# Kernel tuning notes

Measured on AMD Instinct MI355X. Metric: run time of the kernel, lower is better.

## Reference

```python
import math
import jax, jax.numpy as jnp
import numpy as np

D_MODEL, N_HEADS, QKV, D_HEAD, D_FF, N_BLOCKS, IN_DIM = 288, 8, 328, 41, 1315, 4, 83
B, S = 1024, 128
EPS = 1e-5


def setup_inputs() -> dict:
    key = jax.random.key(0)
    ks = iter(jax.random.split(key, 64))
    def rn(shape, scale=0.05):
        return jax.random.normal(next(ks), shape, jnp.float32) * scale
    inp = {
        "x": jax.random.normal(next(ks), (B, S, IN_DIM), jnp.float32),
        "Wp": rn((D_MODEL, IN_DIM)), "bp": rn((D_MODEL,)),
        "phase": rn((D_MODEL,)),
        "Wq": rn((N_BLOCKS, QKV, D_MODEL)), "bq": rn((N_BLOCKS, QKV)),
        "Wk": rn((N_BLOCKS, QKV, D_MODEL)), "bk": rn((N_BLOCKS, QKV)),
        "Wv": rn((N_BLOCKS, QKV, D_MODEL)), "bv": rn((N_BLOCKS, QKV)),
        "Wo": rn((N_BLOCKS, D_MODEL, QKV)), "bo": rn((N_BLOCKS, D_MODEL)),
        "temp": jnp.ones((N_BLOCKS,), jnp.float32) + rn((N_BLOCKS,), 0.01),
        "qscale": jnp.ones((N_BLOCKS, N_HEADS), jnp.float32) + rn((N_BLOCKS, N_HEADS), 0.01),
        "Wf1": rn((N_BLOCKS, D_FF, D_MODEL)), "bf1": rn((N_BLOCKS, D_FF)),
        "Wf2": rn((N_BLOCKS, D_MODEL, D_FF)), "bf2": rn((N_BLOCKS, D_MODEL)),
        "n1w": jnp.ones((N_BLOCKS, D_MODEL), jnp.float32), "n1b": jnp.zeros((N_BLOCKS, D_MODEL), jnp.float32),
        "n2w": jnp.ones((N_BLOCKS, D_MODEL), jnp.float32), "n2b": jnp.zeros((N_BLOCKS, D_MODEL), jnp.float32),
        "skip": jnp.ones((N_BLOCKS,), jnp.float32),
        "bn_w": jnp.ones((D_MODEL,), jnp.float32), "bn_b": jnp.zeros((D_MODEL,), jnp.float32),
        "bn_mean": rn((D_MODEL,)), "bn_var": jax.random.uniform(next(ks), (D_MODEL,), jnp.float32, 0.5, 1.5),
        "h1w": rn((144, D_MODEL)), "h1b": rn((144,)),
        "h2w": rn((72, 144)), "h2b": rn((72,)),
        "h3w": rn((1, 72)), "h3b": rn((1,)),
        "u1w": rn((72, D_MODEL)), "u1b": rn((72,)),
        "u2w": rn((1, 72)), "u2b": rn((1,)),
    }
    return inp


def _layer_norm(x, w, b):
    mu = jnp.mean(x, axis=-1, keepdims=True)
    var = jnp.mean((x - mu) ** 2, axis=-1, keepdims=True)
    return (x - mu) * jax.lax.rsqrt(var + EPS) * w + b


def reference(x, Wp, bp, phase, Wq, bq, Wk, bk, Wv, bv, Wo, bo, temp, qscale,
              Wf1, bf1, Wf2, bf2, n1w, n1b, n2w, n2b, skip,
              bn_w, bn_b, bn_mean, bn_var,
              h1w, h1b, h2w, h2b, h3w, h3b, u1w, u1b, u2w, u2b):
    Bsz, Sl, _ = x.shape
    # input projection
    h = jnp.einsum('bsi,di->bsd', x, Wp) + bp
    # sinusoidal positional encoding modulated by cos(quantum_phase)
    pos = jnp.arange(Sl, dtype=jnp.float32)[:, None]
    div = jnp.exp(jnp.arange(0, D_MODEL, 2, dtype=jnp.float32) * (-math.log(10000.0) / D_MODEL))
    pe = jnp.zeros((Sl, D_MODEL), jnp.float32)
    pe = pe.at[:, 0::2].set(jnp.sin(pos * div)).at[:, 1::2].set(jnp.cos(pos * div))
    h = h + pe * jnp.cos(phase)

    for l in range(N_BLOCKS):
        # attention with temperature-scaled softmax + post-softmax per-head scale
        q = (jnp.einsum('bsd,qd->bsq', h, Wq[l]) + bq[l]).reshape(Bsz, Sl, N_HEADS, D_HEAD)
        k = (jnp.einsum('bsd,qd->bsq', h, Wk[l]) + bk[l]).reshape(Bsz, Sl, N_HEADS, D_HEAD)
        v = (jnp.einsum('bsd,qd->bsq', h, Wv[l]) + bv[l]).reshape(Bsz, Sl, N_HEADS, D_HEAD)
        scale = math.sqrt(D_HEAD) * temp[l]
        scores = jnp.einsum('bqhd,bkhd->bhqk', q, k) / scale  # [B,H,S,S]
        attn = jax.nn.softmax(scores, axis=-1) * qscale[l][None, :, None, None]
        o = jnp.einsum('bhqk,bkhd->bqhd', attn, v).reshape(Bsz, Sl, QKV)
        o = jnp.einsum('bsq,dq->bsd', o, Wo[l]) + bo[l]
        h = _layer_norm(h + skip[l] * o, n1w[l], n1b[l])
        # GELU FFN (exact erf gelu, dropout inactive in eval)
        f = jax.nn.gelu(jnp.einsum('bsd,fd->bsf', h, Wf1[l]) + bf1[l], approximate=False)
        f = jnp.einsum('bsf,df->bsd', f, Wf2[l]) + bf2[l]
        h = _layer_norm(h + f, n2w[l], n2b[l])

    pooled = jnp.mean(h, axis=1)  # [B, D_MODEL]
    # output head: BatchNorm1d (eval, running stats) -> GELU -> MLP
    z = (pooled - bn_mean) * jax.lax.rsqrt(bn_var + EPS) * bn_w + bn_b
    z = jax.nn.gelu(z, approximate=False)
    z = jax.nn.gelu(z @ h1w.T + h1b, approximate=False)
    z = jax.nn.gelu(z @ h2w.T + h2b, approximate=False)
    pred = z @ h3w.T + h3b  # [B, 1]
    # uncertainty head
    u = jax.nn.relu(pooled @ u1w.T + u1b)
    unc = jax.nn.softplus(u @ u2w.T + u2b)  # [B, 1]
    return pred, unc
```

## Files before the change

### kernel.cpp

```cpp
#include <hip/hip_runtime.h>
#include <cstdint>

typedef __attribute__((ext_vector_type(8))) short short8;
typedef __attribute__((ext_vector_type(4))) short s4v;
typedef __attribute__((ext_vector_type(4))) float floatx4;

#define DEV __device__ __forceinline__

DEV short f2bf(float f) {
  unsigned u = __builtin_bit_cast(unsigned, f);
  u += 0x7fffu + ((u >> 16) & 1u);
  return (short)(u >> 16);
}
DEV short f2bf_ru(float f) {
  unsigned u = __builtin_bit_cast(unsigned, f);
  return (short)((u + 0x8000u) >> 16);
}
DEV float bf2f(short s) {
  unsigned u = ((unsigned)(unsigned short)s) << 16;
  return __builtin_bit_cast(float, u);
}
DEV float gelu_exact(float x) {
  return 0.5f * x * (1.0f + erff(x * 0.70710678118654752f));
}
DEV float gelu_fast(float x) {
  const float t2 = 1.5957691216057308f * (x + 0.044715f * x * x * x);
  return x / (1.0f + __expf(-t2));
}
DEV void gload16(const void* g, void* l) {
  __builtin_amdgcn_global_load_lds((const __attribute__((address_space(1))) void*)g,
                                   (__attribute__((address_space(3))) void*)l,
                                   16, 0, 0);
}

template<int MODE>
__global__ __launch_bounds__(256)
void gemm_kernel(const short* __restrict__ A, const short* __restrict__ Bw,
                 const float* __restrict__ bias, short* __restrict__ C,
                 const float* __restrict__ pe,
                 int K, int lda, int ldb, int ldc, int Nstore, int NT, long hstride)
{
  __shared__ __align__(16) short lds[128 * 136];
  short* Ct = lds;

  const int tid  = threadIdx.x;
  const int wave = tid >> 6, lane = tid & 63;
  const int quad = lane >> 4, r16 = lane & 15;
  const int per = gridDim.x >> 3;
  const int gti = (blockIdx.x & 7) * per + (blockIdx.x >> 3);
  const int mt = gti / NT, nt = gti - mt * NT;
  const int wm = (wave >> 1) * 64, wn = (wave & 1) * 64;

  const long Abase = (long)mt * 128 * lda;
  const long Bbase = (long)nt * 128 * ldb;

  floatx4 acc[4][4] = {};

  int k0 = 0;
  for (; k0 + 64 <= K; k0 += 64) {
    __syncthreads();
#pragma unroll
    for (int j = 0; j < 8; ++j) {
      const int c2 = tid + j * 256;
      const int op = c2 >> 10;
      const int cb = c2 & 1023;
      const int half = cb >> 9;
      const int sub = cb & 511;
      const int row = sub >> 2, cc = (sub & 3) ^ ((row >> 1) & 3);
      const short* src = op ? (Bw + Bbase + (long)row * ldb + k0 + half * 32 + cc * 8)
                            : (A  + Abase + (long)row * lda + k0 + half * 32 + cc * 8);
      gload16(src, &lds[(size_t)(op * 8192 + half * 4096 + (sub & ~63) * 8)]);
    }
    __syncthreads();

#pragma unroll
    for (int s = 0; s < 2; ++s) {
      short8 af[4], bfr[4];
#pragma unroll
      for (int i = 0; i < 4; ++i) {
        const int R = wm + i * 16 + r16;
        af[i] = *(const short8*)&lds[s * 4096 + R * 32 + (quad ^ ((R >> 1) & 3)) * 8];
      }
#pragma unroll
      for (int j = 0; j < 4; ++j) {
        const int R = wn + j * 16 + r16;
        bfr[j] = *(const short8*)&lds[8192 + s * 4096 + R * 32 + (quad ^ ((R >> 1) & 3)) * 8];
      }
#pragma unroll
      for (int i = 0; i < 4; ++i)
#pragma unroll
        for (int j = 0; j < 4; ++j)
          acc[i][j] = __builtin_amdgcn_mfma_f32_16x16x32_bf16(bfr[j], af[i], acc[i][j], 0, 0, 0);
    }
  }

  if (k0 < K) {
    short* As = lds;
    short* Bs = lds + 128 * 32;
    const int row0 = tid >> 2,         cc0 = (tid & 3) ^ ((row0 >> 1) & 3);
    const int row1 = (256 + tid) >> 2, cc1 = ((256 + tid) & 3) ^ ((row1 >> 1) & 3);
    __syncthreads();
    gload16(A  + Abase + (long)row0 * lda + k0 + cc0 * 8, &As[(0 * 256 + wave * 64) * 8]);
    gload16(A  + Abase + (long)row1 * lda + k0 + cc1 * 8, &As[(1 * 256 + wave * 64) * 8]);
    gload16(Bw + Bbase + (long)row0 * ldb + k0 + cc0 * 8, &Bs[(0 * 256 + wave * 64) * 8]);
    gload16(Bw + Bbase + (long)row1 * ldb + k0 + cc1 * 8, &Bs[(1 * 256 + wave * 64) * 8]);
    __syncthreads();

    short8 af[4], bfr[4];
#pragma unroll
    for (int i = 0; i < 4; ++i) {
      const int R = wm + i * 16 + r16;
      af[i] = *(const short8*)&As[R * 32 + (quad ^ ((R >> 1) & 3)) * 8];
    }
#pragma unroll
    for (int j = 0; j < 4; ++j) {
      const int R = wn + j * 16 + r16;
      bfr[j] = *(const short8*)&Bs[R * 32 + (quad ^ ((R >> 1) & 3)) * 8];
    }
#pragma unroll
    for (int i = 0; i < 4; ++i)
#pragma unroll
      for (int j = 0; j < 4; ++j)
        acc[i][j] = __builtin_amdgcn_mfma_f32_16x16x32_bf16(bfr[j], af[i], acc[i][j], 0, 0, 0);
  }

  const int mb0 = mt * 128, tb = nt * 128;

  __syncthreads();
#pragma unroll
  for (int j = 0; j < 4; ++j) {
    const int n0 = wn + j * 16 + quad * 4;
    const floatx4 b4 = *(const floatx4*)&bias[tb + n0];
#pragma unroll
    for (int i = 0; i < 4; ++i) {
      const int m = wm + i * 16 + r16;
      floatx4 v = acc[i][j] + b4;
      if (MODE == 1) {
#pragma unroll
        for (int rg = 0; rg < 4; ++rg) v[rg] = gelu_fast(v[rg]);
      }
      if (MODE == 2) {
        const floatx4 p4 = *(const floatx4*)&pe[((mb0 + m) & 127) * 384 + tb + n0];
        v = v + p4;
      }
      s4v o4;
#pragma unroll
      for (int rg = 0; rg < 4; ++rg) o4[rg] = f2bf_ru(v[rg]);
      *(s4v*)&Ct[m * 136 + n0] = o4;
    }
  }
  __syncthreads();

#pragma unroll
  for (int rr = 0; rr < 8; ++rr) {
    const int chunk = rr * 256 + tid;
    const int row = chunk >> 4, ch = chunk & 15;
    const int gcol = tb + ch * 8;
    if (MODE == 3) {
      const int g = gcol / 48, d0 = gcol - g * 48;
      *(short8*)(C + (long)g * hstride + (long)(mb0 + row) * 48 + d0) =
          *(const short8*)&Ct[row * 136 + ch * 8];
    } else if (gcol < Nstore) {
      *(short8*)(C + (long)(mb0 + row) * ldc + gcol) = *(const short8*)&Ct[row * 136 + ch * 8];
    }
  }
}

template<bool AHEAD>
__global__ __launch_bounds__(512, 4)
void gemm_ln_kernel(const short* __restrict__ A, const short* __restrict__ Bw,
                    const float* __restrict__ bias, short* __restrict__ h,
                    const float* __restrict__ lnw, const float* __restrict__ lnb,
                    const float* __restrict__ skip_p, int layer, int use_skip,
                    int K, int lda, int ldb, long ahs)
{
  __shared__ __align__(16) short lds[128 * 296];
  __shared__ float redp[4][2][2][16];
  __shared__ float reds[4][2][2][16];
  short* Hs = lds;

  const int tid  = threadIdx.x;
  const int wave = tid >> 6, lane = tid & 63;
  const int quad = lane >> 4, r16 = lane & 15;
  const int wr = wave >> 1, wc = wave & 1;
  const int mt = blockIdx.x;
  const long mrow0 = (long)mt * 128;

  floatx4 acc[2][9] = {};

  auto stage = [&](short* buf, int k0) {
    for (int c = tid; c < 1664; c += 512) {
      const void* src;
      if (c < 512) {
        const int row = c >> 2, cc = (c & 3) ^ ((row >> 1) & 3);
        if (AHEAD) {
          const int kc = k0 + cc * 8;
          const int g = kc / 48, d = kc - g * 48;
          src = A + (long)g * ahs + (mrow0 + row) * 48 + d;
        } else {
          src = A + (mrow0 + row) * lda + k0 + cc * 8;
        }
      } else {
        const int cb = c - 512;
        const int row = cb >> 2, cc = (cb & 3) ^ ((row >> 1) & 3);
        src = Bw + (long)row * ldb + k0 + cc * 8;
      }
      gload16(src, &buf[(size_t)(c & ~63) * 8]);
    }
  };

  auto compute = [&](const short* buf) {
    const short* As_ = buf;
    const short* Bs_ = buf + 4096;
    const int Ra0 = wr * 32 + r16, Ra1 = Ra0 + 16;
    const short8 af0 = *(const short8*)&As_[Ra0 * 32 + (quad ^ ((Ra0 >> 1) & 3)) * 8];
    const short8 af1 = *(const short8*)&As_[Ra1 * 32 + (quad ^ ((Ra1 >> 1) & 3)) * 8];
#pragma unroll
    for (int t = 0; t < 9; ++t) {
      const int Rb = wc * 144 + t * 16 + r16;
      const short8 b = *(const short8*)&Bs_[Rb * 32 + (quad ^ ((Rb >> 1) & 3)) * 8];
      acc[0][t] = __builtin_amdgcn_mfma_f32_16x16x32_bf16(b, af0, acc[0][t], 0, 0, 0);
      acc[1][t] = __builtin_amdgcn_mfma_f32_16x16x32_bf16(b, af1, acc[1][t], 0, 0, 0);
    }
  };

  short* const B0 = lds;
  short* const B1 = lds + 13312;

  stage(B0, 0);
  __syncthreads();
  int k0 = 0;
  while (true) {
    if (k0 + 32 < K) stage(B1, k0 + 32);
    compute(B0);
    __syncthreads();
    k0 += 32;
    if (k0 >= K) break;
    if (k0 + 32 < K) stage(B0, k0 + 32);
    compute(B1);
    __syncthreads();
    k0 += 32;
    if (k0 >= K) break;
  }

  for (int c = tid; c < 4608; c += 512) {
    const int row = c / 36, ch = c - row * 36;
    *(short8*)&Hs[row * 296 + ch * 8] =
        *(const short8*)(h + (mrow0 + row) * 288 + ch * 8);
  }
  __syncthreads();

  const float skipv = use_skip ? skip_p[layer] : 1.0f;
  const int m0 = wr * 32 + r16, m1 = m0 + 16;

  float ps0 = 0.f, ss0 = 0.f, ps1 = 0.f, ss1 = 0.f;
#pragma unroll
  for (int t = 0; t < 9; ++t) {
    const int n0 = wc * 144 + t * 16 + quad * 4;
    const floatx4 b4 = *(const floatx4*)&bias[n0];
    const s4v h40 = *(const s4v*)&Hs[m0 * 296 + n0];
    const s4v h41 = *(const s4v*)&Hs[m1 * 296 + n0];
#pragma unroll
    for (int rg = 0; rg < 4; ++rg) {
      const float y0 = bf2f(h40[rg]) + skipv * (acc[0][t][rg] + b4[rg]);
      const float y1 = bf2f(h41[rg]) + skipv * (acc[1][t][rg] + b4[rg]);
      acc[0][t][rg] = y0; acc[1][t][rg] = y1;
      ps0 += y0; ss0 += y0 * y0;
      ps1 += y1; ss1 += y1 * y1;
    }
  }
  ps0 += __shfl_xor(ps0, 16); ps0 += __shfl_xor(ps0, 32);
  ss0 += __shfl_xor(ss0, 16); ss0 += __shfl_xor(ss0, 32);
  ps1 += __shfl_xor(ps1, 16); ps1 += __shfl_xor(ps1, 32);
  ss1 += __shfl_xor(ss1, 16); ss1 += __shfl_xor(ss1, 32);
  if (lane < 16) {
    redp[wr][wc][0][r16] = ps0; redp[wr][wc][1][r16] = ps1;
    reds[wr][wc][0][r16] = ss0; reds[wr][wc][1][r16] = ss1;
  }
  __syncthreads();
  const float psum0 = redp[wr][0][0][r16] + redp[wr][1][0][r16];
  const float psum1 = redp[wr][0][1][r16] + redp[wr][1][1][r16];
  const float ssum0 = reds[wr][0][0][r16] + reds[wr][1][0][r16];
  const float ssum1 = reds[wr][0][1][r16] + reds[wr][1][1][r16];
  const float mean0 = psum0 * (1.f / 288.f), mean1 = psum1 * (1.f / 288.f);
  const float rstd0 = rsqrtf(ssum0 * (1.f / 288.f) - mean0 * mean0 + 1e-5f);
  const float rstd1 = rsqrtf(ssum1 * (1.f / 288.f) - mean1 * mean1 + 1e-5f);

#pragma unroll
  for (int t = 0; t < 9; ++t) {
    const int n0 = wc * 144 + t * 16 + quad * 4;
    const floatx4 w4 = *(const floatx4*)&lnw[n0];
    const floatx4 l4 = *(const floatx4*)&lnb[n0];
    s4v o0, o1;
#pragma unroll
    for (int rg = 0; rg < 4; ++rg) {
      o0[rg] = f2bf_ru((acc[0][t][rg] - mean0) * rstd0 * w4[rg] + l4[rg]);
      o1[rg] = f2bf_ru((acc[1][t][rg] - mean1) * rstd1 * w4[rg] + l4[rg]);
    }
    *(s4v*)&Hs[m0 * 296 + n0] = o0;
    *(s4v*)&Hs[m1 * 296 + n0] = o1;
  }
  __syncthreads();

  for (int c = tid; c < 4608; c += 512) {
    const int row = c / 36, ch = c - row * 36;
    *(short8*)(h + (mrow0 + row) * 288 + ch * 8) =
        *(const short8*)&Hs[row * 296 + ch * 8];
  }
}

__global__ __launch_bounds__(512, 2)
void ffn_kernel(short* __restrict__ h,
                const short* __restrict__ W1, const float* __restrict__ b1,
                const short* __restrict__ W2, const float* __restrict__ b2,
                const float* __restrict__ lnw, const float* __restrict__ lnb)
{
  __shared__ __align__(16) short lds[53248];
  __shared__ float redp[4][2][2][16];
  __shared__ float reds[4][2][2][16];
  short* const fl = lds + 36864;

  const int tid  = threadIdx.x;
  const int wave = tid >> 6, lane = tid & 63;
  const int quad = lane >> 4, r16 = lane & 15;
  const int wr = wave >> 1, wp = wave & 1;
  const long mrow0 = (long)blockIdx.x * 128;

  short8 ha[2][9];
#pragma unroll
  for (int i = 0; i < 2; ++i) {
    const long rb = (mrow0 + wr * 32 + i * 16 + r16) * 288L;
#pragma unroll
    for (int k9 = 0; k9 < 9; ++k9)
      ha[i][k9] = *(const short8*)(h + rb + k9 * 32 + quad * 8);
  }

  floatx4 acc2[2][9] = {};

  auto stageW1_128 = [&](int c, int kb, short* dst) {
#pragma unroll
    for (int j = 0; j < 4; ++j) {
      const int c2t = tid + j * 512;
      const int s = c2t >> 9, c2 = c2t & 511;
      const int row = c2 >> 2, cc = (c2 & 3) ^ ((row >> 1) & 3);
      gload16(W1 + ((long)(c * 128 + row)) * 288 + kb + s * 32 + cc * 8,
              &dst[(size_t)(s * 4096 + (c2 & ~63) * 8)]);
    }
  };
  auto stageW1_32 = [&](int c, short* dst) {
    const int row = tid >> 2, cc = (tid & 3) ^ ((row >> 1) & 3);
    gload16(W1 + ((long)(c * 128 + row)) * 288 + 256 + cc * 8,
            &dst[(size_t)(tid & ~63) * 8]);
  };
  auto stageW2_64 = [&](int c, int kb, short* dst) {
    for (int c2t = tid; c2t < 2304; c2t += 512) {
      const int s = (c2t >= 1152) ? 1 : 0;
      const int c2 = c2t - s * 1152;
      const int row = c2 >> 2, cc = (c2 & 3) ^ ((row >> 1) & 3);
      gload16(W2 + (long)row * 1408 + c * 128 + kb + s * 32 + cc * 8,
              &dst[(size_t)(s * 9216 + (c2 & ~63) * 8)]);
    }
  };

  short* const ring0 = lds;
  short* const ring1 = lds + 18432;

  stageW1_128(0, 0, ring0);
  __syncthreads();
  int cur = 0;

  for (int c = 0; c < 11; ++c) {
    floatx4 acc1[2][4] = {};

    auto g1_128 = [&](const short* Sc, int hb) {
#pragma unroll
      for (int s = 0; s < 4; ++s) {
        short8 bfr[4];
#pragma unroll
        for (int j = 0; j < 4; ++j) {
          const int R = wp * 64 + j * 16 + r16;
          bfr[j] = *(const short8*)&Sc[s * 4096 + R * 32 + (quad ^ ((R >> 1) & 3)) * 8];
        }
#pragma unroll
        for (int i = 0; i < 2; ++i)
#pragma unroll
          for (int j = 0; j < 4; ++j)
            acc1[i][j] = __builtin_amdgcn_mfma_f32_16x16x32_bf16(bfr[j], ha[i][hb + s], acc1[i][j], 0, 0, 0);
      }
    };

    {
      short* const Sn = cur ? ring0 : ring1;
      const short* Sc = cur ? ring1 : ring0;
      stageW1_128(c, 128, Sn);
      g1_128(Sc, 0);
      __syncthreads();
      cur ^= 1;
    }
    {
      short* const Sn = cur ? ring0 : ring1;
      const short* Sc = cur ? ring1 : ring0;
      stageW1_32(c, Sn);
      g1_128(Sc, 4);
      __syncthreads();
      cur ^= 1;
    }
    {
      short* const Sn = cur ? ring0 : ring1;
      const short* Sc = cur ? ring1 : ring0;
      stageW2_64(c, 0, Sn);

      short8 bfr[4];
#pragma unroll
      for (int j = 0; j < 4; ++j) {
        const int R = wp * 64 + j * 16 + r16;
        bfr[j] = *(const short8*)&Sc[R * 32 + (quad ^ ((R >> 1) & 3)) * 8];
      }
#pragma unroll
      for (int i = 0; i < 2; ++i)
#pragma unroll
        for (int j = 0; j < 4; ++j)
          acc1[i][j] = __builtin_amdgcn_mfma_f32_16x16x32_bf16(bfr[j], ha[i][8], acc1[i][j], 0, 0, 0);

#pragma unroll
      for (int i = 0; i < 2; ++i) {
        const int m = wr * 32 + i * 16 + r16;
#pragma unroll
        for (int j = 0; j < 4; ++j) {
          const int nb = c * 128 + wp * 64 + j * 16 + quad * 4;
          const floatx4 b4 = *(const floatx4*)&b1[nb];
          s4v o;
#pragma unroll
          for (int rg = 0; rg < 4; ++rg)
            o[rg] = f2bf_ru(gelu_fast(acc1[i][j][rg] + b4[rg]));
          const int ks = wp * 2 + (j >> 1);
          const int mg = ((j & 1) * 2 + (quad >> 1)) ^ ((m >> 1) & 3);
          *(s4v*)&fl[ks * 4096 + m * 32 + mg * 8 + (quad & 1) * 4] = o;
        }
      }
      __syncthreads();
      cur ^= 1;
    }
#pragma unroll
    for (int g2t = 0; g2t < 2; ++g2t) {
      short* const Sn = cur ? ring0 : ring1;
      const short* Sc = cur ? ring1 : ring0;
      if (g2t == 0)    stageW2_64(c, 64, Sn);
      else if (c < 10) stageW1_128(c + 1, 0, Sn);

#pragma unroll
      for (int s = 0; s < 2; ++s) {
        const int ks = g2t * 2 + s;
        short8 af2[2];
#pragma unroll
        for (int i = 0; i < 2; ++i) {
          const int R = wr * 32 + i * 16 + r16;
          af2[i] = *(const short8*)&fl[ks * 4096 + R * 32 + (quad ^ ((R >> 1) & 3)) * 8];
        }
        short8 br[9];
#pragma unroll
        for (int t = 0; t < 9; ++t) {
          const int R = wp * 144 + t * 16 + r16;
          br[t] = *(const short8*)&Sc[s * 9216 + R * 32 + (quad ^ ((R >> 1) & 3)) * 8];
        }
#pragma unroll
        for (int i = 0; i < 2; ++i)
#pragma unroll
          for (int t = 0; t < 9; ++t)
            acc2[i][t] = __builtin_amdgcn_mfma_f32_16x16x32_bf16(br[t], af2[i], acc2[i][t], 0, 0, 0);
      }
      __syncthreads();
      cur ^= 1;
    }
  }

  for (int c2 = tid; c2 < 4608; c2 += 512) {
    const int row = c2 / 36, ch = c2 - row * 36;
    *(short8*)&lds[row * 296 + ch * 8] =
        *(const short8*)(h + (mrow0 + row) * 288 + ch * 8);
  }
  __syncthreads();

  const int m0 = wr * 32 + r16, m1 = m0 + 16;
  float ps0 = 0.f, ss0 = 0.f, ps1 = 0.f, ss1 = 0.f;
#pragma unroll
  for (int t = 0; t < 9; ++t) {
    const int n0 = wp * 144 + t * 16 + quad * 4;
    const floatx4 b4 = *(const floatx4*)&b2[n0];
    const s4v h40 = *(const s4v*)&lds[m0 * 296 + n0];
    const s4v h41 = *(const s4v*)&lds[m1 * 296 + n0];
#pragma unroll
    for (int rg = 0; rg < 4; ++rg) {
      const float y0 = bf2f(h40[rg]) + acc2[0][t][rg] + b4[rg];
      const float y1 = bf2f(h41[rg]) + acc2[1][t][rg] + b4[rg];
      acc2[0][t][rg] = y0; acc2[1][t][rg] = y1;
      ps0 += y0; ss0 += y0 * y0;
      ps1 += y1; ss1 += y1 * y1;
    }
  }
  ps0 += __shfl_xor(ps0, 16); ps0 += __shfl_xor(ps0, 32);
  ss0 += __shfl_xor(ss0, 16); ss0 += __shfl_xor(ss0, 32);
  ps1 += __shfl_xor(ps1, 16); ps1 += __shfl_xor(ps1, 32);
  ss1 += __shfl_xor(ss1, 16); ss1 += __shfl_xor(ss1, 32);
  if (lane < 16) {
    redp[wr][wp][0][r16] = ps0; redp[wr][wp][1][r16] = ps1;
    reds[wr][wp][0][r16] = ss0; reds[wr][wp][1][r16] = ss1;
  }
  __syncthreads();
  const float psum0 = redp[wr][0][0][r16] + redp[wr][1][0][r16];
  const float psum1 = redp[wr][0][1][r16] + redp[wr][1][1][r16];
  const float ssum0 = reds[wr][0][0][r16] + reds[wr][1][0][r16];
  const float ssum1 = reds[wr][0][1][r16] + reds[wr][1][1][r16];
  const float mean0 = psum0 * (1.f / 288.f), mean1 = psum1 * (1.f / 288.f);
  const float rstd0 = rsqrtf(ssum0 * (1.f / 288.f) - mean0 * mean0 + 1e-5f);
  const float rstd1 = rsqrtf(ssum1 * (1.f / 288.f) - mean1 * mean1 + 1e-5f);

#pragma unroll
  for (int t = 0; t < 9; ++t) {
    const int n0 = wp * 144 + t * 16 + quad * 4;
    const floatx4 w4 = *(const floatx4*)&lnw[n0];
    const floatx4 l4 = *(const floatx4*)&lnb[n0];
    s4v o0, o1;
#pragma unroll
    for (int rg = 0; rg < 4; ++rg) {
      o0[rg] = f2bf_ru((acc2[0][t][rg] - mean0) * rstd0 * w4[rg] + l4[rg]);
      o1[rg] = f2bf_ru((acc2[1][t][rg] - mean1) * rstd1 * w4[rg] + l4[rg]);
    }
    *(s4v*)&lds[m0 * 296 + n0] = o0;
    *(s4v*)&lds[m1 * 296 + n0] = o1;
  }
  __syncthreads();

  for (int c2 = tid; c2 < 4608; c2 += 512) {
    const int row = c2 / 36, ch = c2 - row * 36;
    *(short8*)(h + (mrow0 + row) * 288 + ch * 8) =
        *(const short8*)&lds[row * 296 + ch * 8];
  }
}

__global__ __launch_bounds__(256)
void attn_kernel(short* __restrict__ qkv,
                 const float* __restrict__ qscale, int layer, long Mc)
{
  __shared__ __align__(16) short qk[2 * 128 * 72];
  __shared__ __align__(16) short vsT[48 * 136 + 32];
  __shared__ float red[2][2][64];

  short* qs = qk;
  short* ks = qk + 128 * 72;
  short* Pb = qk;

  const int b = blockIdx.x, h = blockIdx.y;
  const int tid = threadIdx.x;
  const long sec = Mc * 48;
  const short* qg = qkv + (long)h * sec + (long)b * 128 * 48;
  const short* kg = qg + 8 * sec;
  const short* vg = qg + 16 * sec;
  short* og = qkv + (long)(16 + h) * sec + (long)b * 128 * 48;

  for (int c = tid; c < 768; c += 256) {
    const int s = c / 6, dc = c - (c / 6) * 6;
    *(short8*)&qs[s * 72 + dc * 8] = *(const short8*)(qg + (long)s * 48 + dc * 8);
    *(short8*)&ks[s * 72 + dc * 8] = *(const short8*)(kg + (long)s * 48 + dc * 8);
  }
  {
    short8 z;
#pragma unroll
    for (int j = 0; j < 8; ++j) z[j] = 0;
    for (int c = tid; c < 384; c += 256) {
      const int s = c / 3, t = c - (c / 3) * 3;
      *(short8*)&qs[s * 72 + 48 + t * 8] = z;
      *(short8*)&ks[s * 72 + 48 + t * 8] = z;
    }
  }
  for (int c = tid; c < 768; c += 256) {
    const int s = c & 127, dc = c >> 7;
    const short8 tv = *(const short8*)(vg + (long)s * 48 + dc * 8);
#pragma unroll
    for (int j = 0; j < 8; ++j) {
      const int row = dc * 8 + j;
      vsT[row * 136 + ((row >> 3) & 3) * 8 + s] = tv[j];
    }
  }
  __syncthreads();

  const int wave = tid >> 6, lane = tid & 63;
  const int quad = lane >> 4, r16 = lane & 15;
  const int wm = (wave >> 1) * 64, wn = (wave & 1) * 64;
  const int rh = wave >> 1, ch = wave & 1;
  const float qsc = qscale[layer * 8 + h];

  floatx4 acc[4][4] = {};
#pragma unroll
  for (int kk = 0; kk < 2; ++kk) {
    const int k0 = kk * 32;
    short8 af[4], bfr[4];
#pragma unroll
    for (int i = 0; i < 4; ++i)
      af[i] = *(const short8*)&qs[(wm + i * 16 + r16) * 72 + k0 + quad * 8];
#pragma unroll
    for (int j = 0; j < 4; ++j)
      bfr[j] = *(const short8*)&ks[(wn + j * 16 + r16) * 72 + k0 + quad * 8];
#pragma unroll
    for (int i = 0; i < 4; ++i)
#pragma unroll
      for (int j = 0; j < 4; ++j)
        acc[i][j] = __builtin_amdgcn_mfma_f32_16x16x32_bf16(bfr[j], af[i], acc[i][j], 0, 0, 0);
  }

  float rmax[4], rsum[4];
#pragma unroll
  for (int i = 0; i < 4; ++i) {
    float m = acc[i][0][0];
#pragma unroll
    for (int j = 0; j < 4; ++j)
#pragma unroll
      for (int rg = 0; rg < 4; ++rg) m = fmaxf(m, acc[i][j][rg]);
    m = fmaxf(m, __shfl_xor(m, 16));
    m = fmaxf(m, __shfl_xor(m, 32));
    rmax[i] = m;
  }
  if (lane < 16)
#pragma unroll
    for (int i = 0; i < 4; ++i) red[rh][ch][i * 16 + r16] = rmax[i];
  __syncthreads();
#pragma unroll
  for (int i = 0; i < 4; ++i)
    rmax[i] = fmaxf(red[rh][0][i * 16 + r16], red[rh][1][i * 16 + r16]);

#pragma unroll
  for (int i = 0; i < 4; ++i) {
    float s = 0.f;
#pragma unroll
    for (int j = 0; j < 4; ++j)
#pragma unroll
      for (int rg = 0; rg < 4; ++rg) {
        const float e = __expf(acc[i][j][rg] - rmax[i]);
        acc[i][j][rg] = e;
        s += e;
      }
    s += __shfl_xor(s, 16);
    s += __shfl_xor(s, 32);
    rsum[i] = s;
  }
  __syncthreads();
  if (lane < 16)
#pragma unroll
    for (int i = 0; i < 4; ++i) red[rh][ch][i * 16 + r16] = rsum[i];
  __syncthreads();
#pragma unroll
  for (int i = 0; i < 4; ++i)
    rmax[i] = qsc / (red[rh][0][i * 16 + r16] + red[rh][1][i * 16 + r16]);

#pragma unroll
  for (int i = 0; i < 4; ++i) {
    const int sq = wm + i * 16 + r16;
#pragma unroll
    for (int j = 0; j < 4; ++j) {
      const int sk0 = wn + j * 16 + quad * 4;
      s4v p4;
#pragma unroll
      for (int rg = 0; rg < 4; ++rg) p4[rg] = f2bf_ru(acc[i][j][rg] * rmax[i]);
      *(s4v*)&Pb[sq * 136 + sk0] = p4;
    }
  }
  __syncthreads();

  const int om = (wave >> 1) * 64, on = (wave & 1) * 32;
  const int jn = (on == 0) ? 2 : 1;
  floatx4 oacc[4][2] = {};
  for (int kk = 0; kk < 4; ++kk) {
    const int k0 = kk * 32;
    short8 af[4], bfr[2];
#pragma unroll
    for (int i = 0; i < 4; ++i)
      af[i] = *(const short8*)&Pb[(om + i * 16 + r16) * 136 + k0 + quad * 8];
    for (int j = 0; j < jn; ++j) {
      const int row = on + j * 16 + r16;
      bfr[j] = *(const short8*)&vsT[row * 136 + ((row >> 3) & 3) * 8 + k0 + quad * 8];
    }
#pragma unroll
    for (int i = 0; i < 4; ++i)
      for (int j = 0; j < jn; ++j)
        oacc[i][j] = __builtin_amdgcn_mfma_f32_16x16x32_bf16(bfr[j], af[i], oacc[i][j], 0, 0, 0);
  }
#pragma unroll
  for (int i = 0; i < 4; ++i)
    for (int j = 0; j < jn; ++j) {
      const int d0 = on + j * 16 + quad * 4;
      const int sq = om + i * 16 + r16;
      s4v o4;
#pragma unroll
      for (int rg = 0; rg < 4; ++rg) o4[rg] = f2bf_ru(oacc[i][j][rg]);
      *(s4v*)(og + (long)sq * 48 + d0) = o4;
    }
}

__global__ __launch_bounds__(256)
void head_kernel(const short* __restrict__ hb, float* __restrict__ out,
                 const float* bn_w, const float* bn_b, const float* bn_mean, const float* bn_var,
                 const float* h1w, const float* h1b, const float* h2w, const float* h2b,
                 const float* h3w, const float* h3b,
                 const float* u1w, const float* u1b, const float* u2w, const float* u2b)
{
  __shared__ float psum[252][8];
  __shared__ float pooled[288], z[288], z1[144], z2[72], uu[72];
  const int b = blockIdx.x, tid = threadIdx.x;

  if (tid < 252) {
    const int cch = tid % 36, grp = tid / 36;
    float a[8];
#pragma unroll
    for (int j = 0; j < 8; ++j) a[j] = 0.f;
    for (int r = grp; r < 128; r += 7) {
      const short8 hv = *(const short8*)(hb + ((long)b * 128 + r) * 288 + cch * 8);
#pragma unroll
      for (int j = 0; j < 8; ++j) a[j] += bf2f(hv[j]);
    }
#pragma unroll
    for (int j = 0; j < 8; ++j) psum[tid][j] = a[j];
  }
  __syncthreads();
  for (int d = tid; d < 288; d += 256) {
    const int cch = d >> 3, j = d & 7;
    float s = 0.f;
#pragma unroll
    for (int g = 0; g < 7; ++g) s += psum[g * 36 + cch][j];
    pooled[d] = s * (1.f / 128.f);
  }
  __syncthreads();

  for (int d = tid; d < 288; d += 256) {
    const float p = pooled[d];
    z[d] = gelu_exact((p - bn_mean[d]) * rsqrtf(bn_var[d] + 1e-5f) * bn_w[d] + bn_b[d]);
  }
  __syncthreads();

  if (tid < 144) {
    float s = h1b[tid];
    for (int k = 0; k < 288; ++k) s += z[k] * h1w[tid * 288 + k];
    z1[tid] = gelu_exact(s);
  } else if (tid < 216) {
    const int t = tid - 144;
    float s = u1b[t];
    for (int k = 0; k < 288; ++k) s += pooled[k] * u1w[t * 288 + k];
    uu[t] = fmaxf(s, 0.f);
  }
  __syncthreads();

  if (tid < 72) {
    float s = h2b[tid];
    for (int k = 0; k < 144; ++k) s += z1[k] * h2w[tid * 144 + k];
    z2[tid] = gelu_exact(s);
  }
  __syncthreads();

  if (tid == 0) {
    float s = h3b[0];
    for (int k = 0; k < 72; ++k) s += z2[k] * h3w[k];
    out[b] = s;
  }
  if (tid == 64) {
    float s = u2b[0];
    for (int k = 0; k < 72; ++k) s += uu[k] * u2w[k];
    out[1024 + b] = (s > 20.f) ? s : log1pf(__expf(s));
  }
}

__global__ void conv_w_kernel(const float* __restrict__ src, short* __restrict__ dst,
                              int N, int K, int Npad, int Kpad, int total)
{
  const int i = blockIdx.x * 256 + threadIdx.x;
  if (i >= total) return;
  const int kk = i % Kpad;
  const int t  = i / Kpad;
  const int n  = t % Npad;
  const int l  = t / Npad;
  const float v = (n < N && kk < K) ? src[((long)l * N + n) * K + kk] : 0.f;
  dst[i] = f2bf(v);
}

__global__ void conv_b_kernel(const float* __restrict__ src, float* __restrict__ dst,
                              int N, int Npad, int total)
{
  const int i = blockIdx.x * 256 + threadIdx.x;
  if (i >= total) return;
  const int n = i % Npad, l = i / Npad;
  dst[i] = (n < N) ? src[l * N + n] : 0.f;
}

__global__ void conv_wqkv_kernel(const float* __restrict__ Wq, const float* __restrict__ Wk,
                                 const float* __restrict__ Wv, const float* __restrict__ temp,
                                 short* __restrict__ dst)
{
  const int i = blockIdx.x * 256 + threadIdx.x;
  if (i >= 4 * 1152 * 288) return;
  const int kk = i % 288;
  const int t  = i / 288;
  const int r  = t % 1152;
  const int l  = t / 1152;
  const int g  = r / 48, d = r - (r / 48) * 48;
  const int sec = g >> 3, head = g & 7;
  float v = 0.f;
  if (d < 41) {
    const float* W = (sec == 0) ? Wq : (sec == 1) ? Wk : Wv;
    v = W[((long)l * 328 + head * 41 + d) * 288 + kk];
    if (sec == 0) v *= 1.0f / (6.4031242374328485f * temp[l]);
  }
  dst[i] = f2bf(v);
}

__global__ void conv_bqkv_kernel(const float* __restrict__ bq, const float* __restrict__ bk,
                                 const float* __restrict__ bv, const float* __restrict__ temp,
                                 float* __restrict__ dst)
{
  const int i = blockIdx.x * 256 + threadIdx.x;
  if (i >= 4 * 1152) return;
  const int r = i % 1152, l = i / 1152;
  const int g = r / 48, d = r - (r / 48) * 48;
  const int sec = g >> 3, head = g & 7;
  float v = 0.f;
  if (d < 41) {
    const float* b = (sec == 0) ? bq : (sec == 1) ? bk : bv;
    v = b[l * 328 + head * 41 + d];
    if (sec == 0) v *= 1.0f / (6.4031242374328485f * temp[l]);
  }
  dst[i] = v;
}

__global__ void conv_wo_kernel(const float* __restrict__ Wo, short* __restrict__ dst)
{
  const int i = blockIdx.x * 256 + threadIdx.x;
  if (i >= 4 * 288 * 384) return;
  const int kk = i % 384;
  const int t  = i / 384;
  const int n  = t % 288;
  const int l  = t / 288;
  const int head = kk / 48, d = kk - head * 48;
  float v = 0.f;
  if (d < 41) v = Wo[((long)l * 288 + n) * 328 + head * 41 + d];
  dst[i] = f2bf(v);
}

__global__ void conv_x_kernel(const float* __restrict__ x, short* __restrict__ xb, int total)
{
  const int i = blockIdx.x * 256 + threadIdx.x;
  if (i >= total) return;
  const int c = i % 96;
  const int r = i / 96;
  xb[i] = f2bf((c < 83) ? x[(long)r * 83 + c] : 0.f);
}

__global__ void pe_kernel(const float* __restrict__ phase, float* __restrict__ pe_mod)
{
  const int i = blockIdx.x * 256 + threadIdx.x;
  if (i >= 128 * 384) return;
  const int d = i % 384, s = i / 384;
  float out = 0.f;
  if (d < 288) {
    const int pair = d >> 1;
    const float divv = expf((float)(2 * pair) * (-9.210340371976184f / 288.f));
    const float arg = (float)s * divv;
    const float v = (d & 1) ? cosf(arg) : sinf(arg);
    out = v * cosf(phase[d]);
  }
  pe_mod[i] = out;
}

extern "C" void kernel_launch(void* const* d_in, const int* in_sizes, int n_in,
                              void* d_out, int out_size, void* d_ws, size_t ws_size,
                              hipStream_t stream)
{
  (void)in_sizes; (void)n_in; (void)out_size;

  const float* x     = (const float*)d_in[0];
  const float* Wp    = (const float*)d_in[1];
  const float* bp    = (const float*)d_in[2];
  const float* phase = (const float*)d_in[3];
  const float* Wq    = (const float*)d_in[4];
  const float* bq    = (const float*)d_in[5];
  const float* Wk    = (const float*)d_in[6];
  const float* bk    = (const float*)d_in[7];
  const float* Wv    = (const float*)d_in[8];
  const float* bv    = (const float*)d_in[9];
  const float* Wo    = (const float*)d_in[10];
  const float* bo    = (const float*)d_in[11];
  const float* temp  = (const float*)d_in[12];
  const float* qscale= (const float*)d_in[13];
  const float* Wf1   = (const float*)d_in[14];
  const float* bf1   = (const float*)d_in[15];
  const float* Wf2   = (const float*)d_in[16];
  const float* bf2   = (const float*)d_in[17];
  const float* n1w   = (const float*)d_in[18];
  const float* n1b   = (const float*)d_in[19];
  const float* n2w   = (const float*)d_in[20];
  const float* n2b   = (const float*)d_in[21];
  const float* skip  = (const float*)d_in[22];
  const float* bn_w  = (const float*)d_in[23];
  const float* bn_b  = (const float*)d_in[24];
  const float* bn_mean=(const float*)d_in[25];
  const float* bn_var= (const float*)d_in[26];
  const float* h1w   = (const float*)d_in[27];
  const float* h1b   = (const float*)d_in[28];
  const float* h2w   = (const float*)d_in[29];
  const float* h2b   = (const float*)d_in[30];
  const float* h3w   = (const float*)d_in[31];
  const float* h3b   = (const float*)d_in[32];
  const float* u1w   = (const float*)d_in[33];
  const float* u1b   = (const float*)d_in[34];
  const float* u2w   = (const float*)d_in[35];
  const float* u2b   = (const float*)d_in[36];

  char* ws = (char*)d_ws;
  size_t off = 0;
  auto alloc = [&](size_t n) -> char* {
    off = (off + 255) & ~(size_t)255;
    char* p = ws + off;
    off += n;
    return p;
  };

  const long M = 131072;

  short* h_bf   = (short*)alloc((size_t)M * 288 * 2);
  float* pe_mod = (float*)alloc(128 * 384 * 4);

  short* Wp_b   = (short*)alloc((size_t)384 * 96 * 2);
  short* Wqkv_b = (short*)alloc((size_t)4 * 1152 * 288 * 2);
  short* Wo_b   = (short*)alloc((size_t)4 * 288 * 384 * 2);
  short* Wf1_b  = (short*)alloc((size_t)4 * 1408 * 288 * 2);
  short* Wf2_b  = (short*)alloc((size_t)4 * 384 * 1408 * 2);

  float* bp_p   = (float*)alloc((size_t)384 * 4);
  float* bqkv_p = (float*)alloc((size_t)4 * 1152 * 4);
  float* bo_p   = (float*)alloc((size_t)4 * 384 * 4);
  float* bf1_p  = (float*)alloc((size_t)4 * 1408 * 4);
  float* bf2_p  = (float*)alloc((size_t)4 * 384 * 4);

  const size_t fixed = off;
  int NC = 1;
  while (NC < 16 && fixed + (size_t)(M / NC) * 2304 + (1u << 20) > ws_size) NC <<= 1;
  const long Mc = M / NC;
  const long sec = Mc * 48;

  char* R = alloc((size_t)Mc * 2304);
  short* qkv_bf = (short*)R;
  short* x_bfc  = (short*)R;

  const dim3 blk(256);

  auto conv_w = [&](const float* s, short* d, int N, int K, int Np, int Kp, int L) {
    const int total = L * Np * Kp;
    conv_w_kernel<<<dim3((total + 255) / 256), blk, 0, stream>>>(s, d, N, K, Np, Kp, total);
  };
  auto conv_b = [&](const float* s, float* d, int N, int Np, int L) {
    const int total = L * Np;
    conv_b_kernel<<<dim3((total + 255) / 256), blk, 0, stream>>>(s, d, N, Np, total);
  };
  conv_w(Wp,  Wp_b,  288,   83, 384,   96, 1);
  conv_wqkv_kernel<<<dim3((4 * 1152 * 288 + 255) / 256), blk, 0, stream>>>(Wq, Wk, Wv, temp, Wqkv_b);
  conv_wo_kernel<<<dim3((4 * 288 * 384 + 255) / 256), blk, 0, stream>>>(Wo, Wo_b);
  conv_w(Wf1, Wf1_b, 1315, 288, 1408, 288, 4);
  conv_w(Wf2, Wf2_b, 288, 1315, 384, 1408, 4);
  conv_b(bp,  bp_p,  288,  384, 1);
  conv_bqkv_kernel<<<dim3((4 * 1152 + 255) / 256), blk, 0, stream>>>(bq, bk, bv, temp, bqkv_p);
  conv_b(bo,  bo_p,  288,  384, 4);
  conv_b(bf1, bf1_p, 1315, 1408, 4);
  conv_b(bf2, bf2_p, 288,  384, 4);
  pe_kernel<<<dim3((128 * 384 + 255) / 256), blk, 0, stream>>>(phase, pe_mod);

  auto gemm = [&](int mode, const short* A, const short* Bmat, const float* bias,
                  short* C, const float* pe, int K, int lda, int ldb, int ldc,
                  int Nstore, int NT, long Mrows, long hstride) {
    const dim3 grid((unsigned)((Mrows / 128) * NT));
    switch (mode) {
      case 0: gemm_kernel<0><<<grid, blk, 0, stream>>>(A, Bmat, bias, C, pe, K, lda, ldb, ldc, Nstore, NT, hstride); break;
      case 1: gemm_kernel<1><<<grid, blk, 0, stream>>>(A, Bmat, bias, C, pe, K, lda, ldb, ldc, Nstore, NT, hstride); break;
      case 2: gemm_kernel<2><<<grid, blk, 0, stream>>>(A, Bmat, bias, C, pe, K, lda, ldb, ldc, Nstore, NT, hstride); break;
      default: gemm_kernel<3><<<grid, blk, 0, stream>>>(A, Bmat, bias, C, pe, K, lda, ldb, ldc, Nstore, NT, hstride); break;
    }
  };

  for (int c = 0; c < NC; ++c) {
    const float* x_c = x + (size_t)c * Mc * 83;
    short* h_c = h_bf + (size_t)c * Mc * 288;

    const int xtot = (int)(Mc * 96);
    conv_x_kernel<<<dim3((xtot + 255) / 256), blk, 0, stream>>>(x_c, x_bfc, xtot);

    gemm(2, x_bfc, Wp_b, bp_p, h_c, pe_mod, 96, 96, 96, 288, 288, 3, Mc, 0);

    for (int l = 0; l < 4; ++l) {
      const short* Wqkv_l = Wqkv_b + (size_t)l * 1152 * 288;
      const short* Wo_l   = Wo_b   + (size_t)l * 288 * 384;
      const short* Wf1_l  = Wf1_b  + (size_t)l * 1408 * 288;
      const short* Wf2_l  = Wf2_b  + (size_t)l * 384 * 1408;

      gemm(3, h_c, Wqkv_l, bqkv_p + l * 1152, qkv_bf, nullptr,
           288, 288, 288, 0, 1152, 9, Mc, sec);

      attn_kernel<<<dim3((unsigned)(Mc / 128), 8), blk, 0, stream>>>(
          qkv_bf, qscale, l, Mc);

      gemm_ln_kernel<true><<<dim3((unsigned)(Mc / 128)), dim3(512), 0, stream>>>(
          qkv_bf + 16 * sec, Wo_l, bo_p + l * 384, h_c, n1w + l * 288, n1b + l * 288,
          skip, l, 1, 384, 48, 384, sec);

      ffn_kernel<<<dim3((unsigned)(Mc / 128)), dim3(512), 0, stream>>>(
          h_c, Wf1_l, bf1_p + l * 1408, Wf2_l, bf2_p + l * 384,
          n2w + l * 288, n2b + l * 288);
    }
  }

  head_kernel<<<dim3(1024), blk, 0, stream>>>(h_bf, (float*)d_out,
      bn_w, bn_b, bn_mean, bn_var,
      h1w, h1b, h2w, h2b, h3w, h3b,
      u1w, u1b, u2w, u2b);
}
```

Measured before the change: 3.066 ms.

## Replace FFN syncthreads with partial vmcnt waits to overlap weight staging

Replaces the full __syncthreads in the FFN kernel's double-buffered weight staging with explicit s_waitcnt vmcnt(N) plus s_barrier, so the barrier waits only for the previous stage's async global-to-LDS loads. The next stage's loads stay in flight during the MFMA compute. It also unrolls the W2 staging loop to a fixed five loads (wrapping duplicates) so the vmcnt counts are exact, and caches the b1 bias in LDS. The risk is that any miscount of outstanding loads gives a data race.

```diff
diff --git a/kernel.cpp b/kernel.cpp
--- a/kernel.cpp
+++ b/kernel.cpp
@@ -316,6 +316,7 @@
                 const float* __restrict__ lnw, const float* __restrict__ lnb)
 {
   __shared__ __align__(16) short lds[53248];
+  __shared__ __align__(16) float b1s[1408];
   __shared__ float redp[4][2][2][16];
   __shared__ float reds[4][2][2][16];
   short* const fl = lds + 36864;
@@ -334,6 +335,8 @@
     for (int k9 = 0; k9 < 9; ++k9)
       ha[i][k9] = *(const short8*)(h + rb + k9 * 32 + quad * 8);
   }
+
+  for (int i = tid; i < 1408; i += 512) b1s[i] = b1[i];
 
   floatx4 acc2[2][9] = {};
 
@@ -353,7 +356,10 @@
             &dst[(size_t)(tid & ~63) * 8]);
   };
   auto stageW2_64 = [&](int c, int kb, short* dst) {
-    for (int c2t = tid; c2t < 2304; c2t += 512) {
+#pragma unroll
+    for (int j = 0; j < 5; ++j) {
+      int c2t = tid + j * 512;
+      if (c2t >= 2304) c2t -= 2304;
       const int s = (c2t >= 1152) ? 1 : 0;
       const int c2 = c2t - s * 1152;
       const int row = c2 >> 2, cc = (c2 & 3) ^ ((row >> 1) & 3);
@@ -366,7 +372,9 @@
   short* const ring1 = lds + 18432;
 
   stageW1_128(0, 0, ring0);
-  __syncthreads();
+  asm volatile("s_waitcnt lgkmcnt(0)" ::: "memory");
+  asm volatile("s_barrier" ::: "memory");
+  __builtin_amdgcn_sched_barrier(0);
   int cur = 0;
 
   for (int c = 0; c < 11; ++c) {
@@ -393,22 +401,35 @@
       short* const Sn = cur ? ring0 : ring1;
       const short* Sc = cur ? ring1 : ring0;
       stageW1_128(c, 128, Sn);
+      asm volatile("s_waitcnt vmcnt(4)" ::: "memory");
+      asm volatile("s_barrier" ::: "memory");
+      __builtin_amdgcn_sched_barrier(0);
       g1_128(Sc, 0);
-      __syncthreads();
+      asm volatile("s_waitcnt lgkmcnt(0)" ::: "memory");
+      asm volatile("s_barrier" ::: "memory");
+      __builtin_amdgcn_sched_barrier(0);
       cur ^= 1;
     }
     {
       short* const Sn = cur ? ring0 : ring1;
       const short* Sc = cur ? ring1 : ring0;
       stageW1_32(c, Sn);
+      asm volatile("s_waitcnt vmcnt(1)" ::: "memory");
+      asm volatile("s_barrier" ::: "memory");
+      __builtin_amdgcn_sched_barrier(0);
       g1_128(Sc, 4);
-      __syncthreads();
+      asm volatile("s_waitcnt lgkmcnt(0)" ::: "memory");
+      asm volatile("s_barrier" ::: "memory");
+      __builtin_amdgcn_sched_barrier(0);
       cur ^= 1;
     }
     {
       short* const Sn = cur ? ring0 : ring1;
       const short* Sc = cur ? ring1 : ring0;
       stageW2_64(c, 0, Sn);
+      asm volatile("s_waitcnt vmcnt(5)" ::: "memory");
+      asm volatile("s_barrier" ::: "memory");
+      __builtin_amdgcn_sched_barrier(0);
 
       short8 bfr[4];
 #pragma unroll
@@ -428,7 +449,7 @@
 #pragma unroll
         for (int j = 0; j < 4; ++j) {
           const int nb = c * 128 + wp * 64 + j * 16 + quad * 4;
-          const floatx4 b4 = *(const floatx4*)&b1[nb];
+          const floatx4 b4 = *(const floatx4*)&b1s[nb];
           s4v o;
 #pragma unroll
           for (int rg = 0; rg < 4; ++rg)
@@ -438,15 +459,26 @@
           *(s4v*)&fl[ks * 4096 + m * 32 + mg * 8 + (quad & 1) * 4] = o;
         }
       }
-      __syncthreads();
+      asm volatile("s_waitcnt lgkmcnt(0)" ::: "memory");
+      asm volatile("s_barrier" ::: "memory");
+      __builtin_amdgcn_sched_barrier(0);
       cur ^= 1;
     }
 #pragma unroll
     for (int g2t = 0; g2t < 2; ++g2t) {
       short* const Sn = cur ? ring0 : ring1;
       const short* Sc = cur ? ring1 : ring0;
-      if (g2t == 0)    stageW2_64(c, 64, Sn);
-      else if (c < 10) stageW1_128(c + 1, 0, Sn);
+      if (g2t == 0) {
+        stageW2_64(c, 64, Sn);
+        asm volatile("s_waitcnt vmcnt(5)" ::: "memory");
+      } else if (c < 10) {
+        stageW1_128(c + 1, 0, Sn);
+        asm volatile("s_waitcnt vmcnt(4)" ::: "memory");
+      } else {
+        asm volatile("s_waitcnt vmcnt(0)" ::: "memory");
+      }
+      asm volatile("s_barrier" ::: "memory");
+      __builtin_amdgcn_sched_barrier(0);
 
 #pragma unroll
       for (int s = 0; s < 2; ++s) {
@@ -469,7 +501,9 @@
           for (int t = 0; t < 9; ++t)
             acc2[i][t] = __builtin_amdgcn_mfma_f32_16x16x32_bf16(br[t], af2[i], acc2[i][t], 0, 0, 0);
       }
-      __syncthreads();
+      asm volatile("s_waitcnt lgkmcnt(0)" ::: "memory");
+      asm volatile("s_barrier" ::: "memory");
+      __builtin_amdgcn_sched_barrier(0);
       cur ^= 1;
     }
   }
```

New measurement: 3.390 ms. +10.6%, slower.
